# Kernel optimization log

Measured on AMD Instinct MI355X. Metric: run time of the kernel, lower is better.

Reference implementation:

```python
import jax, jax.numpy as jnp
import numpy as np

EPS = 1e-06
N, K, O = 100000, 64, 1024


def setup_inputs() -> dict:
    key = jax.random.key(0)
    k1, k2, k3 = jax.random.split(key, 3)
    # counts: non-negative read counts per particle (scaled uniform, like count data)
    counts = jnp.floor(jax.random.uniform(k1, (N, O), dtype=jnp.float32) * 10.0)
    # otu_dist: K community profiles over O OTUs (simplex rows)
    otu_raw = jax.random.uniform(k2, (K, O), dtype=jnp.float32) + 1e-3
    otu_dist = otu_raw / otu_raw.sum(axis=-1, keepdims=True)
    # comm_dist: mixture weights over K communities (simplex)
    comm_raw = jax.random.uniform(k3, (K,), dtype=jnp.float32) + 1e-3
    comm_dist = comm_raw / comm_raw.sum()
    return {"counts": counts, "otu_dist": otu_dist, "comm_dist": comm_dist}


def reference(counts, otu_dist, comm_dist):
    # (counts[:,None,:] * log(otu_dist[None,:,:]+EPS)).sum(-1) == counts @ log(otu_dist+EPS).T
    # (N,K) per-particle per-community log-likelihood + log prior weight
    log_otu = jnp.log(otu_dist + EPS)                      # (K, O)
    logsumexpand = jnp.einsum('no,ko->nk', counts, log_otu) + jnp.log(comm_dist + EPS)[None, :]
    summand = jax.scipy.special.logsumexp(logsumexpand, axis=1)  # (N,)
    return summand.sum()
```

## Files before the change

kernel.cpp:

```cpp
#include <hip/hip_runtime.h>
#include <hip/hip_bf16.h>
#include <math.h>

#define NP 100000
#define KC 64
#define OD 1024
#define EPSF 1e-6f

#define ROWS_PER_BLOCK 128
#define NBLOCKS ((NP + ROWS_PER_BLOCK - 1) / ROWS_PER_BLOCK)

typedef __attribute__((ext_vector_type(8))) short short8;
typedef __attribute__((ext_vector_type(4))) float f32x4;

#define WS_LOGW      0
#define WS_PARTIALS  256
#define WS_BSTAGE    8192

__device__ __forceinline__ unsigned short f32_bf16_rn(float f) {
  unsigned int u = __float_as_uint(f);
  unsigned int r = u + 0x7fffu + ((u >> 16) & 1u);
  return (unsigned short)(r >> 16);
}

__global__ void prep_kernel(const float* __restrict__ otu,
                            const float* __restrict__ comm,
                            unsigned short* __restrict__ bstage,
                            float* __restrict__ logw) {
  int b = blockIdx.x;
  if (b < KC) {
    int c = b & 15, ct = b >> 4;
    for (int k = threadIdx.x; k < OD; k += blockDim.x) {
      float x = logf(otu[b * OD + k] + EPSF);
      unsigned short h = f32_bf16_rn(x);
      float hf = __uint_as_float(((unsigned int)h) << 16);
      unsigned short l = f32_bf16_rn(x - hf);
      int kb = k >> 5, g = (k >> 3) & 3, kk = k & 7;
      size_t base = (size_t)kb * 4096 + (size_t)ct * 512
                  + (size_t)(g * 16 + c) * 8 + kk;
      bstage[base] = h;
      bstage[base + 2048] = l;
    }
  } else {
    if (threadIdx.x < KC) logw[threadIdx.x] = logf(comm[threadIdx.x] + EPSF);
  }
}

__global__ __launch_bounds__(256, 2)
void ll_kernel(const float* __restrict__ counts,
               const unsigned short* __restrict__ bstage,
               const float* __restrict__ logw,
               double* __restrict__ partials) {
  const int tid = threadIdx.x;
  const int wave = tid >> 6;
  const int lane = tid & 63;
  const int g = lane >> 4;
  const int c = lane & 15;
  const int rowBase = blockIdx.x * ROWS_PER_BLOCK + wave * 32;

  f32x4 acc[2][4];
#pragma unroll
  for (int i = 0; i < 2; ++i)
#pragma unroll
    for (int j = 0; j < 4; ++j)
      acc[i][j] = (f32x4){0.f, 0.f, 0.f, 0.f};

  int r0 = rowBase + c;      if (r0 >= NP) r0 = NP - 1;
  int r1 = rowBase + 16 + c; if (r1 >= NP) r1 = NP - 1;
  const float* pa0 = counts + (size_t)r0 * OD + g * 8;
  const float* pa1 = counts + (size_t)r1 * OD + g * 8;

  const int p = blockIdx.x & 3;

  for (int ci = 0; ci < 4; ++ci) {
    const int t = (p + ci) & 3;
    const float* a0 = pa0 + t * 256;
    const float* a1 = pa1 + t * 256;

    float4 x0[8], x1[8], y0[8], y1[8];
#pragma unroll
    for (int s = 0; s < 8; ++s) {
      x0[s] = *(const float4*)(a0 + s * 32);
      x1[s] = *(const float4*)(a0 + s * 32 + 4);
      y0[s] = *(const float4*)(a1 + s * 32);
      y1[s] = *(const float4*)(a1 + s * 32 + 4);
    }

    short8 ah0[8], ah1[8];
#pragma unroll
    for (int s = 0; s < 8; ++s) {
      union { unsigned int u[4]; short8 v; } u0, u1;
      u0.u[0] = __builtin_amdgcn_perm(__float_as_uint(x0[s].y), __float_as_uint(x0[s].x), 0x07060302u);
      u0.u[1] = __builtin_amdgcn_perm(__float_as_uint(x0[s].w), __float_as_uint(x0[s].z), 0x07060302u);
      u0.u[2] = __builtin_amdgcn_perm(__float_as_uint(x1[s].y), __float_as_uint(x1[s].x), 0x07060302u);
      u0.u[3] = __builtin_amdgcn_perm(__float_as_uint(x1[s].w), __float_as_uint(x1[s].z), 0x07060302u);
      u1.u[0] = __builtin_amdgcn_perm(__float_as_uint(y0[s].y), __float_as_uint(y0[s].x), 0x07060302u);
      u1.u[1] = __builtin_amdgcn_perm(__float_as_uint(y0[s].w), __float_as_uint(y0[s].z), 0x07060302u);
      u1.u[2] = __builtin_amdgcn_perm(__float_as_uint(y1[s].y), __float_as_uint(y1[s].x), 0x07060302u);
      u1.u[3] = __builtin_amdgcn_perm(__float_as_uint(y1[s].w), __float_as_uint(y1[s].z), 0x07060302u);
      ah0[s] = u0.v;
      ah1[s] = u1.v;
    }

#pragma unroll
    for (int s = 0; s < 8; ++s) {
      const int kb = t * 8 + s;
      const unsigned short* bb = bstage + (size_t)kb * 4096 + (size_t)lane * 8;
      short8 fbh[4], fbl[4];
#pragma unroll
      for (int ct = 0; ct < 4; ++ct) {
        fbh[ct] = *(const short8*)(bb + ct * 512);
        fbl[ct] = *(const short8*)(bb + 2048 + ct * 512);
      }
#pragma unroll
      for (int ct = 0; ct < 4; ++ct) {
        acc[0][ct] = __builtin_amdgcn_mfma_f32_16x16x32_bf16(ah0[s], fbh[ct], acc[0][ct], 0, 0, 0);
        acc[1][ct] = __builtin_amdgcn_mfma_f32_16x16x32_bf16(ah1[s], fbh[ct], acc[1][ct], 0, 0, 0);
        acc[0][ct] = __builtin_amdgcn_mfma_f32_16x16x32_bf16(ah0[s], fbl[ct], acc[0][ct], 0, 0, 0);
        acc[1][ct] = __builtin_amdgcn_mfma_f32_16x16x32_bf16(ah1[s], fbl[ct], acc[1][ct], 0, 0, 0);
      }
    }
  }

  float lw[4];
#pragma unroll
  for (int ct = 0; ct < 4; ++ct) lw[ct] = logw[ct * 16 + c];

  double lsum = 0.0;
#pragma unroll
  for (int rt = 0; rt < 2; ++rt) {
#pragma unroll
    for (int r = 0; r < 4; ++r) {
      float v0 = acc[rt][0][r] + lw[0];
      float v1 = acc[rt][1][r] + lw[1];
      float v2 = acc[rt][2][r] + lw[2];
      float v3 = acc[rt][3][r] + lw[3];
      float m = fmaxf(fmaxf(v0, v1), fmaxf(v2, v3));
      m = fmaxf(m, __shfl_xor(m, 1));
      m = fmaxf(m, __shfl_xor(m, 2));
      m = fmaxf(m, __shfl_xor(m, 4));
      m = fmaxf(m, __shfl_xor(m, 8));
      float s = __expf(v0 - m) + __expf(v1 - m) + __expf(v2 - m) + __expf(v3 - m);
      s += __shfl_xor(s, 1);
      s += __shfl_xor(s, 2);
      s += __shfl_xor(s, 4);
      s += __shfl_xor(s, 8);
      float lse = m + __logf(s);
      int row = rowBase + rt * 16 + g * 4 + r;
      if (c == 0 && row < NP) lsum += (double)lse;
    }
  }
  lsum += __shfl_xor(lsum, 16);
  lsum += __shfl_xor(lsum, 32);

  __shared__ double wpart[4];
  if (lane == 0) wpart[wave] = lsum;
  __syncthreads();
  if (tid == 0) partials[blockIdx.x] = wpart[0] + wpart[1] + wpart[2] + wpart[3];
}

__global__ void finalize_kernel(const double* __restrict__ partials,
                                float* __restrict__ out) {
  double s = 0.0;
  for (int i = threadIdx.x; i < NBLOCKS; i += 256) s += partials[i];
  s += __shfl_xor(s, 1);
  s += __shfl_xor(s, 2);
  s += __shfl_xor(s, 4);
  s += __shfl_xor(s, 8);
  s += __shfl_xor(s, 16);
  s += __shfl_xor(s, 32);
  __shared__ double sp[4];
  int w = threadIdx.x >> 6, lane = threadIdx.x & 63;
  if (lane == 0) sp[w] = s;
  __syncthreads();
  if (threadIdx.x == 0) out[0] = (float)(sp[0] + sp[1] + sp[2] + sp[3]);
}

extern "C" void kernel_launch(void* const* d_in, const int* in_sizes, int n_in,
                              void* d_out, int out_size, void* d_ws, size_t ws_size,
                              hipStream_t stream) {
  const float* counts = (const float*)d_in[0];
  const float* otu    = (const float*)d_in[1];
  const float* comm   = (const float*)d_in[2];
  float* out = (float*)d_out;
  char* ws = (char*)d_ws;

  float* logw          = (float*)(ws + WS_LOGW);
  double* partials     = (double*)(ws + WS_PARTIALS);
  unsigned short* bst  = (unsigned short*)(ws + WS_BSTAGE);

  prep_kernel<<<KC + 1, 256, 0, stream>>>(otu, comm, bst, logw);
  ll_kernel<<<NBLOCKS, 256, 0, stream>>>(counts, bst, logw, partials);
  finalize_kernel<<<1, 256, 0, stream>>>(partials, out);
}
```

Baseline: 564.1 us.

## Stage counts tiles through swizzled LDS with coalesced loads in single-wave blocks

Each block becomes one wave handling 32 rows. The wave loads count rows with fully coalesced float4 loads, converts them to bf16, and writes them into a swizzled LDS buffer. MFMA A-fragments are then read back from LDS, replacing the previous strided per-lane global loads that gathered fragment layouts directly. This is meant to improve global load coalescing and stream the HBM-bound counts read more efficiently. In exchange it adds a 32KB LDS staging step and no longer uses the 4-wave block reduction.

```diff
diff --git a/kernel.cpp b/kernel.cpp
--- a/kernel.cpp
+++ b/kernel.cpp
@@ -7,15 +7,15 @@
 #define OD 1024
 #define EPSF 1e-6f
 
-#define ROWS_PER_BLOCK 128
-#define NBLOCKS ((NP + ROWS_PER_BLOCK - 1) / ROWS_PER_BLOCK)
+#define ROWS_PER_BLOCK 32
+#define NBLK 3125
 
 typedef __attribute__((ext_vector_type(8))) short short8;
 typedef __attribute__((ext_vector_type(4))) float f32x4;
 
 #define WS_LOGW      0
 #define WS_PARTIALS  256
-#define WS_BSTAGE    8192
+#define WS_BSTAGE    32768
 
 __device__ __forceinline__ unsigned short f32_bf16_rn(float f) {
   unsigned int u = __float_as_uint(f);
@@ -46,17 +46,23 @@
   }
 }
 
-__global__ __launch_bounds__(256, 2)
+__global__ __launch_bounds__(64)
 void ll_kernel(const float* __restrict__ counts,
                const unsigned short* __restrict__ bstage,
                const float* __restrict__ logw,
                double* __restrict__ partials) {
-  const int tid = threadIdx.x;
-  const int wave = tid >> 6;
-  const int lane = tid & 63;
-  const int g = lane >> 4;
-  const int c = lane & 15;
-  const int rowBase = blockIdx.x * ROWS_PER_BLOCK + wave * 32;
+  __shared__ unsigned short afrag[16384];
+  char* lds = (char*)afrag;
+  const int lane = threadIdx.x;
+  const int g = lane >> 4, c = lane & 15;
+  const int row0 = blockIdx.x * ROWS_PER_BLOCK;
+  const float* src = counts + (size_t)row0 * OD;
+
+  const int kb3 = lane >> 3;
+  const int gq  = (lane >> 1) & 3;
+  const int hq  = lane & 1;
+  const int cA0 = kb3 * 2048 + gq * 256 + hq * 8;
+  const int cA1 = 16384 + cA0;
 
   f32x4 acc[2][4];
 #pragma unroll
@@ -65,59 +71,54 @@
     for (int j = 0; j < 4; ++j)
       acc[i][j] = (f32x4){0.f, 0.f, 0.f, 0.f};
 
-  int r0 = rowBase + c;      if (r0 >= NP) r0 = NP - 1;
-  int r1 = rowBase + 16 + c; if (r1 >= NP) r1 = NP - 1;
-  const float* pa0 = counts + (size_t)r0 * OD + g * 8;
-  const float* pa1 = counts + (size_t)r1 * OD + g * 8;
+  for (int hf = 0; hf < 2; ++hf) {
+    const float* hsrc = src + hf * 512 + lane * 4;
 
-  const int p = blockIdx.x & 3;
-
-  for (int ci = 0; ci < 4; ++ci) {
-    const int t = (p + ci) & 3;
-    const float* a0 = pa0 + t * 256;
-    const float* a1 = pa1 + t * 256;
-
-    float4 x0[8], x1[8], y0[8], y1[8];
+    float4 fb[4][2];
 #pragma unroll
-    for (int s = 0; s < 8; ++s) {
-      x0[s] = *(const float4*)(a0 + s * 32);
-      x1[s] = *(const float4*)(a0 + s * 32 + 4);
-      y0[s] = *(const float4*)(a1 + s * 32);
-      y1[s] = *(const float4*)(a1 + s * 32 + 4);
+    for (int r = 0; r < 4; ++r) {
+      fb[r][0] = *(const float4*)(hsrc + r * 1024);
+      fb[r][1] = *(const float4*)(hsrc + r * 1024 + 256);
     }
-
-    short8 ah0[8], ah1[8];
 #pragma unroll
-    for (int s = 0; s < 8; ++s) {
-      union { unsigned int u[4]; short8 v; } u0, u1;
-      u0.u[0] = __builtin_amdgcn_perm(__float_as_uint(x0[s].y), __float_as_uint(x0[s].x), 0x07060302u);
-      u0.u[1] = __builtin_amdgcn_perm(__float_as_uint(x0[s].w), __float_as_uint(x0[s].z), 0x07060302u);
-      u0.u[2] = __builtin_amdgcn_perm(__float_as_uint(x1[s].y), __float_as_uint(x1[s].x), 0x07060302u);
-      u0.u[3] = __builtin_amdgcn_perm(__float_as_uint(x1[s].w), __float_as_uint(x1[s].z), 0x07060302u);
-      u1.u[0] = __builtin_amdgcn_perm(__float_as_uint(y0[s].y), __float_as_uint(y0[s].x), 0x07060302u);
-      u1.u[1] = __builtin_amdgcn_perm(__float_as_uint(y0[s].w), __float_as_uint(y0[s].z), 0x07060302u);
-      u1.u[2] = __builtin_amdgcn_perm(__float_as_uint(y1[s].y), __float_as_uint(y1[s].x), 0x07060302u);
-      u1.u[3] = __builtin_amdgcn_perm(__float_as_uint(y1[s].w), __float_as_uint(y1[s].z), 0x07060302u);
-      ah0[s] = u0.v;
-      ah1[s] = u1.v;
+    for (int r = 0; r < 32; ++r) {
+      const int slot = r & 3;
+      const int roff = ((r >> 4) << 10) + (((r & 15) ^ kb3) << 4);
+      {
+        float4 f = fb[slot][0];
+        uint2 w;
+        w.x = __builtin_amdgcn_perm(__float_as_uint(f.y), __float_as_uint(f.x), 0x07060302u);
+        w.y = __builtin_amdgcn_perm(__float_as_uint(f.w), __float_as_uint(f.z), 0x07060302u);
+        *(uint2*)(lds + cA0 + roff) = w;
+        f = fb[slot][1];
+        w.x = __builtin_amdgcn_perm(__float_as_uint(f.y), __float_as_uint(f.x), 0x07060302u);
+        w.y = __builtin_amdgcn_perm(__float_as_uint(f.w), __float_as_uint(f.z), 0x07060302u);
+        *(uint2*)(lds + cA1 + roff) = w;
+      }
+      if (r + 4 < 32) {
+        fb[slot][0] = *(const float4*)(hsrc + (r + 4) * 1024);
+        fb[slot][1] = *(const float4*)(hsrc + (r + 4) * 1024 + 256);
+      }
     }
 
 #pragma unroll
-    for (int s = 0; s < 8; ++s) {
-      const int kb = t * 8 + s;
-      const unsigned short* bb = bstage + (size_t)kb * 4096 + (size_t)lane * 8;
-      short8 fbh[4], fbl[4];
+    for (int kl = 0; kl < 16; ++kl) {
+      const int swz = (c ^ (kl & 7)) << 4;
+      short8 a0 = *(const short8*)(lds + kl * 2048 + g * 256 + swz);
+      short8 a1 = *(const short8*)(lds + kl * 2048 + 1024 + g * 256 + swz);
+      const unsigned short* bb = bstage + (size_t)(hf * 16 + kl) * 4096 + lane * 8;
+      short8 bh[4], bl[4];
 #pragma unroll
       for (int ct = 0; ct < 4; ++ct) {
-        fbh[ct] = *(const short8*)(bb + ct * 512);
-        fbl[ct] = *(const short8*)(bb + 2048 + ct * 512);
+        bh[ct] = *(const short8*)(bb + ct * 512);
+        bl[ct] = *(const short8*)(bb + 2048 + ct * 512);
       }
 #pragma unroll
       for (int ct = 0; ct < 4; ++ct) {
-        acc[0][ct] = __builtin_amdgcn_mfma_f32_16x16x32_bf16(ah0[s], fbh[ct], acc[0][ct], 0, 0, 0);
-        acc[1][ct] = __builtin_amdgcn_mfma_f32_16x16x32_bf16(ah1[s], fbh[ct], acc[1][ct], 0, 0, 0);
-        acc[0][ct] = __builtin_amdgcn_mfma_f32_16x16x32_bf16(ah0[s], fbl[ct], acc[0][ct], 0, 0, 0);
-        acc[1][ct] = __builtin_amdgcn_mfma_f32_16x16x32_bf16(ah1[s], fbl[ct], acc[1][ct], 0, 0, 0);
+        acc[0][ct] = __builtin_amdgcn_mfma_f32_16x16x32_bf16(a0, bh[ct], acc[0][ct], 0, 0, 0);
+        acc[1][ct] = __builtin_amdgcn_mfma_f32_16x16x32_bf16(a1, bh[ct], acc[1][ct], 0, 0, 0);
+        acc[0][ct] = __builtin_amdgcn_mfma_f32_16x16x32_bf16(a0, bl[ct], acc[0][ct], 0, 0, 0);
+        acc[1][ct] = __builtin_amdgcn_mfma_f32_16x16x32_bf16(a1, bl[ct], acc[1][ct], 0, 0, 0);
       }
     }
   }
@@ -146,23 +147,18 @@
       s += __shfl_xor(s, 4);
       s += __shfl_xor(s, 8);
       float lse = m + __logf(s);
-      int row = rowBase + rt * 16 + g * 4 + r;
-      if (c == 0 && row < NP) lsum += (double)lse;
+      if (c == 0) lsum += (double)lse;
     }
   }
   lsum += __shfl_xor(lsum, 16);
   lsum += __shfl_xor(lsum, 32);
-
-  __shared__ double wpart[4];
-  if (lane == 0) wpart[wave] = lsum;
-  __syncthreads();
-  if (tid == 0) partials[blockIdx.x] = wpart[0] + wpart[1] + wpart[2] + wpart[3];
+  if (lane == 0) partials[blockIdx.x] = lsum;
 }
 
 __global__ void finalize_kernel(const double* __restrict__ partials,
                                 float* __restrict__ out) {
   double s = 0.0;
-  for (int i = threadIdx.x; i < NBLOCKS; i += 256) s += partials[i];
+  for (int i = threadIdx.x; i < NBLK; i += 256) s += partials[i];
   s += __shfl_xor(s, 1);
   s += __shfl_xor(s, 2);
   s += __shfl_xor(s, 4);
@@ -190,6 +186,6 @@
   unsigned short* bst  = (unsigned short*)(ws + WS_BSTAGE);
 
   prep_kernel<<<KC + 1, 256, 0, stream>>>(otu, comm, bst, logw);
-  ll_kernel<<<NBLOCKS, 256, 0, stream>>>(counts, bst, logw, partials);
+  ll_kernel<<<NBLK, 64, 0, stream>>>(counts, bst, logw, partials);
   finalize_kernel<<<1, 256, 0, stream>>>(partials, out);
 }
```

Measured after the change: 608.2 us. 1.08x slower.

## Double-buffer counts loads in small groups with nontemporal loads

Applied to the files above, without the earlier changes.

The main loop is restructured from four large chunks, each of which loaded 32 float4 per lane before computing, into sixteen small groups of two k-blocks. Each group's loads are issued while the previous group is computed (ping-pong register buffers), and the counts reads become nontemporal loads. This aims to overlap HBM latency with MFMA work and to cut register pressure, at the cost of fewer loads in flight per wave. The per-block start phase is widened to eight staggered offsets.

```diff
diff --git a/kernel.cpp b/kernel.cpp
--- a/kernel.cpp
+++ b/kernel.cpp
@@ -46,6 +46,51 @@
   }
 }
 
+struct AG { f32x4 x0[2], x1[2], y0[2], y1[2]; };
+
+__device__ __forceinline__ void load_group(AG& b, const float* a0, const float* a1) {
+#pragma unroll
+  for (int s = 0; s < 2; ++s) {
+    b.x0[s] = __builtin_nontemporal_load((const f32x4*)(a0 + s * 32));
+    b.x1[s] = __builtin_nontemporal_load((const f32x4*)(a0 + s * 32 + 4));
+    b.y0[s] = __builtin_nontemporal_load((const f32x4*)(a1 + s * 32));
+    b.y1[s] = __builtin_nontemporal_load((const f32x4*)(a1 + s * 32 + 4));
+  }
+}
+
+__device__ __forceinline__ void compute_group(const AG& b, int ph,
+                                              const unsigned short* __restrict__ bstage,
+                                              int lane, f32x4 (&acc)[2][4]) {
+#pragma unroll
+  for (int s = 0; s < 2; ++s) {
+    union { unsigned int u[4]; short8 v; } u0, u1;
+    u0.u[0] = __builtin_amdgcn_perm(__float_as_uint(b.x0[s].y), __float_as_uint(b.x0[s].x), 0x07060302u);
+    u0.u[1] = __builtin_amdgcn_perm(__float_as_uint(b.x0[s].w), __float_as_uint(b.x0[s].z), 0x07060302u);
+    u0.u[2] = __builtin_amdgcn_perm(__float_as_uint(b.x1[s].y), __float_as_uint(b.x1[s].x), 0x07060302u);
+    u0.u[3] = __builtin_amdgcn_perm(__float_as_uint(b.x1[s].w), __float_as_uint(b.x1[s].z), 0x07060302u);
+    u1.u[0] = __builtin_amdgcn_perm(__float_as_uint(b.y0[s].y), __float_as_uint(b.y0[s].x), 0x07060302u);
+    u1.u[1] = __builtin_amdgcn_perm(__float_as_uint(b.y0[s].w), __float_as_uint(b.y0[s].z), 0x07060302u);
+    u1.u[2] = __builtin_amdgcn_perm(__float_as_uint(b.y1[s].y), __float_as_uint(b.y1[s].x), 0x07060302u);
+    u1.u[3] = __builtin_amdgcn_perm(__float_as_uint(b.y1[s].w), __float_as_uint(b.y1[s].z), 0x07060302u);
+
+    const int kb = ph * 2 + s;
+    const unsigned short* bb = bstage + (size_t)kb * 4096 + (size_t)lane * 8;
+    short8 bh[4], bl[4];
+#pragma unroll
+    for (int ct = 0; ct < 4; ++ct) {
+      bh[ct] = *(const short8*)(bb + ct * 512);
+      bl[ct] = *(const short8*)(bb + 2048 + ct * 512);
+    }
+#pragma unroll
+    for (int ct = 0; ct < 4; ++ct) {
+      acc[0][ct] = __builtin_amdgcn_mfma_f32_16x16x32_bf16(u0.v, bh[ct], acc[0][ct], 0, 0, 0);
+      acc[1][ct] = __builtin_amdgcn_mfma_f32_16x16x32_bf16(u1.v, bh[ct], acc[1][ct], 0, 0, 0);
+      acc[0][ct] = __builtin_amdgcn_mfma_f32_16x16x32_bf16(u0.v, bl[ct], acc[0][ct], 0, 0, 0);
+      acc[1][ct] = __builtin_amdgcn_mfma_f32_16x16x32_bf16(u1.v, bl[ct], acc[1][ct], 0, 0, 0);
+    }
+  }
+}
+
 __global__ __launch_bounds__(256, 2)
 void ll_kernel(const float* __restrict__ counts,
                const unsigned short* __restrict__ bstage,
@@ -70,55 +115,21 @@
   const float* pa0 = counts + (size_t)r0 * OD + g * 8;
   const float* pa1 = counts + (size_t)r1 * OD + g * 8;
 
-  const int p = blockIdx.x & 3;
-
-  for (int ci = 0; ci < 4; ++ci) {
-    const int t = (p + ci) & 3;
-    const float* a0 = pa0 + t * 256;
-    const float* a1 = pa1 + t * 256;
-
-    float4 x0[8], x1[8], y0[8], y1[8];
-#pragma unroll
-    for (int s = 0; s < 8; ++s) {
-      x0[s] = *(const float4*)(a0 + s * 32);
-      x1[s] = *(const float4*)(a0 + s * 32 + 4);
-      y0[s] = *(const float4*)(a1 + s * 32);
-      y1[s] = *(const float4*)(a1 + s * 32 + 4);
-    }
-
-    short8 ah0[8], ah1[8];
-#pragma unroll
-    for (int s = 0; s < 8; ++s) {
-      union { unsigned int u[4]; short8 v; } u0, u1;
-      u0.u[0] = __builtin_amdgcn_perm(__float_as_uint(x0[s].y), __float_as_uint(x0[s].x), 0x07060302u);
-      u0.u[1] = __builtin_amdgcn_perm(__float_as_uint(x0[s].w), __float_as_uint(x0[s].z), 0x07060302u);
-      u0.u[2] = __builtin_amdgcn_perm(__float_as_uint(x1[s].y), __float_as_uint(x1[s].x), 0x07060302u);
-      u0.u[3] = __builtin_amdgcn_perm(__float_as_uint(x1[s].w), __float_as_uint(x1[s].z), 0x07060302u);
-      u1.u[0] = __builtin_amdgcn_perm(__float_as_uint(y0[s].y), __float_as_uint(y0[s].x), 0x07060302u);
-      u1.u[1] = __builtin_amdgcn_perm(__float_as_uint(y0[s].w), __float_as_uint(y0[s].z), 0x07060302u);
-      u1.u[2] = __builtin_amdgcn_perm(__float_as_uint(y1[s].y), __float_as_uint(y1[s].x), 0x07060302u);
-      u1.u[3] = __builtin_amdgcn_perm(__float_as_uint(y1[s].w), __float_as_uint(y1[s].z), 0x07060302u);
-      ah0[s] = u0.v;
-      ah1[s] = u1.v;
-    }
-
-#pragma unroll
-    for (int s = 0; s < 8; ++s) {
-      const int kb = t * 8 + s;
-      const unsigned short* bb = bstage + (size_t)kb * 4096 + (size_t)lane * 8;
-      short8 fbh[4], fbl[4];
-#pragma unroll
-      for (int ct = 0; ct < 4; ++ct) {
-        fbh[ct] = *(const short8*)(bb + ct * 512);
-        fbl[ct] = *(const short8*)(bb + 2048 + ct * 512);
-      }
-#pragma unroll
-      for (int ct = 0; ct < 4; ++ct) {
-        acc[0][ct] = __builtin_amdgcn_mfma_f32_16x16x32_bf16(ah0[s], fbh[ct], acc[0][ct], 0, 0, 0);
-        acc[1][ct] = __builtin_amdgcn_mfma_f32_16x16x32_bf16(ah1[s], fbh[ct], acc[1][ct], 0, 0, 0);
-        acc[0][ct] = __builtin_amdgcn_mfma_f32_16x16x32_bf16(ah0[s], fbl[ct], acc[0][ct], 0, 0, 0);
-        acc[1][ct] = __builtin_amdgcn_mfma_f32_16x16x32_bf16(ah1[s], fbl[ct], acc[1][ct], 0, 0, 0);
-      }
+  const int p0 = (blockIdx.x & 7) << 1;
+
+  AG bA, bB;
+  load_group(bA, pa0 + (size_t)(p0 & 15) * 64, pa1 + (size_t)(p0 & 15) * 64);
+
+#pragma unroll
+  for (int i = 0; i < 16; ++i) {
+    const int ph  = (p0 + i) & 15;
+    const int phn = (p0 + i + 1) & 15;
+    if ((i & 1) == 0) {
+      if (i < 15) load_group(bB, pa0 + (size_t)phn * 64, pa1 + (size_t)phn * 64);
+      compute_group(bA, ph, bstage, lane, acc);
+    } else {
+      if (i < 15) load_group(bA, pa0 + (size_t)phn * 64, pa1 + (size_t)phn * 64);
+      compute_group(bB, ph, bstage, lane, acc);
     }
   }
 
```

Result: slower. 583.2 us (+3.4%).
